# Kernel tuning notes

Measured on AMD Instinct MI355X. Metric: run time of the kernel, lower is better.

The kernel has to match this reference:

```python
import jax, jax.numpy as jnp
import numpy as np

BN_EPS = 1e-5

# Binary_a: sign forward, hard-tanh STE backward (grad zeroed where |x| >= 1)
@jax.custom_vjp
def binary_act(x):
    return jnp.sign(x)

def _ba_fwd(x):
    return jnp.sign(x), x

def _ba_bwd(x, g):
    return (jnp.where((x > -1.0) & (x < 1.0), g, 0.0),)

binary_act.defvjp(_ba_fwd, _ba_bwd)

# Binary_w: sign forward, identity STE backward
@jax.custom_vjp
def binary_w(x):
    return jnp.sign(x)

def _bw_fwd(x):
    return jnp.sign(x), None

def _bw_bwd(_, g):
    return (g,)

binary_w.defvjp(_bw_fwd, _bw_bwd)


def setup_inputs() -> dict:
    key = jax.random.key(0)
    k1, k2, k3 = jax.random.split(key, 3)
    B, Cin, Cout, H, Wd, K = 32, 256, 256, 56, 56, 3
    x = jax.random.normal(k1, (B, Cin, H, Wd), dtype=jnp.float32)
    weight = jax.random.normal(k2, (Cout, Cin, K, K), dtype=jnp.float32) * 0.05
    bias = jax.random.normal(k3, (Cout,), dtype=jnp.float32) * 0.01
    gamma = jnp.ones((Cout,), dtype=jnp.float32)
    beta = jnp.zeros((Cout,), dtype=jnp.float32)
    return {"x": x, "weight": weight, "bias": bias, "gamma": gamma, "beta": beta}


def reference(x, weight, bias, gamma, beta):
    # activation binarization (A=2)
    xb = binary_act(x)
    # weight quantization (W=2): mean-center over in-channel dim, clamp to [-1,1]
    # (done on .data in torch -> values change but no grad through this step)
    wc_val = jnp.clip(weight - jnp.mean(weight, axis=1, keepdims=True), -1.0, 1.0)
    wc = weight + jax.lax.stop_gradient(wc_val - weight)
    # per-output-filter scale alpha = E[|w|] over (in, kh, kw)
    alpha = jnp.mean(jnp.abs(wc), axis=(1, 2, 3), keepdims=True)
    wq = binary_w(wc) * alpha  # [O,I,K,K]
    # conv2d, stride 1, padding 1, groups 1
    y = jax.lax.conv_general_dilated(
        xb, wq, window_strides=(1, 1), padding=((1, 1), (1, 1)),
        dimension_numbers=("NCHW", "OIHW", "NCHW"))
    y = y + bias[None, :, None, None]
    # BatchNorm2d, training-mode forward (biased batch stats)
    mean = jnp.mean(y, axis=(0, 2, 3), keepdims=True)
    var = jnp.mean(jnp.square(y - mean), axis=(0, 2, 3), keepdims=True)
    y = (y - mean) * jax.lax.rsqrt(var + BN_EPS)
    y = y * gamma[None, :, None, None] + beta[None, :, None, None]
    # last_relu=1
    return jax.nn.relu(y)
```

## Files before the change

kernel.cpp:

```cpp
#include <hip/hip_runtime.h>
#include <stdint.h>

typedef unsigned long long u64;
typedef unsigned int u32;
typedef int v4i __attribute__((ext_vector_type(4)));
typedef int v16i __attribute__((ext_vector_type(16)));

#define B_    32
#define CIN   256
#define COUT  256
#define H_    56
#define W_    56
#define HW    3136
#define NPOS  100352
#define HBLK  28
#define NPACKBLK 784


__global__ __launch_bounds__(256) void k_prep(
    const float* __restrict__ x,
    const float* __restrict__ wgt,
    u64* __restrict__ xbits,
    int8_t* __restrict__ Bfrag,
    float* __restrict__ alpha,
    int* __restrict__ ssum,
    unsigned long long* __restrict__ qsum)
{
    const int tid = threadIdx.x;

    if (blockIdx.x < NPACKBLK) {
        const int j = blockIdx.x / 196;
        const int p2 = (blockIdx.x - j * 196) * 256 + tid;
        const int pos0 = p2 * 2;
        const int b = pos0 / HW;
        const int hw = pos0 - b * HW;
        const float* xp = x + (size_t)b * CIN * HW + (size_t)j * 64 * HW + hw;
        u64 b0 = 0, b1 = 0;
#pragma unroll 8
        for (int k = 0; k < 64; ++k) {
            const float2 v = *(const float2*)(xp + (size_t)k * HW);
            b0 |= (u64)(v.x > 0.0f) << k;
            b1 |= (u64)(v.y > 0.0f) << k;
        }
        xbits[(size_t)pos0 * 4 + j] = b0;
        xbits[(size_t)(pos0 + 1) * 4 + j] = b1;
        return;
    }

    const int o = blockIdx.x - NPACKBLK;
    const int i = tid;
    const int wave = i >> 6, lane = i & 63;
    __shared__ float sred[4][12];

    if (i == 0) { ssum[o] = 0; qsum[o] = 0ULL; }

    float w9[9];
#pragma unroll
    for (int t = 0; t < 9; ++t) w9[t] = wgt[(o * 256 + i) * 9 + t];

    float m[9];
#pragma unroll
    for (int t = 0; t < 9; ++t) m[t] = w9[t];
#pragma unroll
    for (int s = 1; s < 64; s <<= 1)
#pragma unroll
        for (int t = 0; t < 9; ++t) m[t] += __shfl_xor(m[t], s, 64);
    if (lane == 0) {
#pragma unroll
        for (int t = 0; t < 9; ++t) sred[wave][t] = m[t];
    }
    __syncthreads();
#pragma unroll
    for (int t = 0; t < 9; ++t)
        m[t] = (sred[0][t] + sred[1][t] + sred[2][t] + sred[3][t]) * (1.0f / 256.0f);

    float wc[9];
    float asum = 0.0f;
#pragma unroll
    for (int t = 0; t < 9; ++t) {
        float v = w9[t] - m[t];
        v = fminf(fmaxf(v, -1.0f), 1.0f);
        wc[t] = v;
        asum += fabsf(v);
    }
#pragma unroll
    for (int s = 1; s < 64; s <<= 1) asum += __shfl_xor(asum, s, 64);
    __syncthreads();
    if (lane == 0) sred[wave][9] = asum;
    __syncthreads();
    if (i == 0)
        alpha[o] = (sred[0][9] + sred[1][9] + sred[2][9] + sred[3][9]) * (1.0f / 2304.0f);

#pragma unroll
    for (int t = 0; t < 9; ++t) {
        const int8_t sv = (wc[t] > 0.0f) ? (int8_t)1 : (int8_t)-1;
        const size_t addr =
            ((size_t)((t * 8 + (i >> 5)) * 8 + (o >> 5)) * 64
             + (size_t)(((i >> 4) & 1) * 32 + (o & 31))) * 16 + (i & 15);
        Bfrag[addr] = sv;
    }
}

#define MFMA_I8(acc, a, b) \
    asm volatile("v_mfma_i32_32x32x32_i8 %0, %1, %2, %0" : "+a"(acc) : "v"(a), "v"(b))

__global__ __launch_bounds__(256, 2) void kc_mfma(
    const u64* __restrict__ xbits,
    const int8_t* __restrict__ Bfrag,
    short* __restrict__ S,
    int* __restrict__ ssum,
    unsigned long long* __restrict__ qsum)
{
    const int blk = blockIdx.x;
    const int b = blk / HBLK;
    const int h0 = (blk - b * HBLK) * 2;
    const int tid = threadIdx.x;

    __shared__ u32 ldsb[4 * 58 * 64];

    for (int it = tid; it < 4 * 58 * 16; it += 256) {
        const int r = it / 928;
        const int rem = it - r * 928;
        const int wp = rem >> 4;
        const int g = rem & 15;
        const int hr = h0 - 1 + r;
        const int w_in = wp - 1;
        const bool inb = (hr >= 0) && (hr < H_) && (w_in >= 0) && (w_in < W_);
        u32 chunk16 = 0;
        if (inb) {
            const u64 word = xbits[((size_t)(b * HW + hr * W_ + w_in)) * 4 + (g >> 2)];
            chunk16 = (u32)(word >> ((g & 3) * 16)) & 0xFFFFu;
        }
        u32 out4[4];
#pragma unroll
        for (int d = 0; d < 4; ++d) {
            const u32 nib = (chunk16 >> (4 * d)) & 0xFu;
            const u32 m1 = (nib * 0x00204081u) & 0x01010101u;
            const u32 inv = m1 ^ 0x01010101u;
            out4[d] = inb ? (0x01010101u ^ (inv * 0xFEu)) : 0u;
        }
        const int gs = (g + wp) & 15;
        u32* dst = &ldsb[((r * 58 + wp) << 6) + gs * 4];
        dst[0] = out4[0]; dst[1] = out4[1]; dst[2] = out4[2]; dst[3] = out4[3];
    }
    __syncthreads();

    const int m0 = tid & 31;
    const int lh = (tid >> 5) & 1;
    const int wv = tid >> 6;
    const int8_t* smem = (const int8_t*)ldsb;
    const int8_t* Bp = Bfrag + (size_t)(tid & 63) * 16;

    auto ldA = [&](int kk, int mt) -> v4i {
        const int tap = kk >> 3, s = kk & 7;
        const int dh = tap / 3;
        const int dw = tap - dh * 3;
        const int r = (mt >> 1) + dh;
        const int wpm = min((mt & 1) * 32 + m0 + dw, 57);
        const int gs = (2 * s + lh + wpm) & 15;
        const int addr = ((r * 58 + wpm) << 8) + (gs << 4);
        return *(const v4i*)(smem + addr);
    };
    auto ldB = [&](int kk, int ntl) -> v4i {
        const size_t off = (size_t)((kk * 8) + wv * 2 + ntl) * 1024;
        return *(const v4i*)(Bp + off);
    };

    v16i acc[4][2] = {};
    v4i A[4][2], Bb[2][2];

#pragma unroll
    for (int mt = 0; mt < 4; ++mt) A[mt][0] = ldA(0, mt);
    Bb[0][0] = ldB(0, 0);
    Bb[1][0] = ldB(0, 1);

#pragma unroll
    for (int kk = 0; kk < 72; ++kk) {
        const int cur = kk & 1, nxt = cur ^ 1;
        if (kk < 71) {
#pragma unroll
            for (int mt = 0; mt < 4; ++mt) A[mt][nxt] = ldA(kk + 1, mt);
            Bb[0][nxt] = ldB(kk + 1, 0);
            Bb[1][nxt] = ldB(kk + 1, 1);
        }
#pragma unroll
        for (int mt = 0; mt < 4; ++mt) {
            MFMA_I8(acc[mt][0], A[mt][cur], Bb[0][cur]);
            MFMA_I8(acc[mt][1], A[mt][cur], Bb[1][cur]);
        }
    }

    asm volatile("s_nop 7\n\ts_nop 7\n\ts_nop 7"
                 : "+a"(acc[0][0]), "+a"(acc[0][1]), "+a"(acc[1][0]), "+a"(acc[1][1]),
                   "+a"(acc[2][0]), "+a"(acc[2][1]), "+a"(acc[3][0]), "+a"(acc[3][1]));

    const int n0 = wv * 64 + m0;
    const int n1 = n0 + 32;
    int s0 = 0, s1 = 0, q0 = 0, q1 = 0;

#pragma unroll
    for (int mt = 0; mt < 4; ++mt) {
        const int h = h0 + (mt >> 1);
        const int rowbase = b * HW + h * W_ + ((mt & 1) << 5);
        const int nval = (mt & 1) ? 12 : 16;
#pragma unroll 16
        for (int reg = 0; reg < nval; ++reg) {
            const int m = (reg & 3) + ((reg >> 2) << 3) + (lh << 2);
            const int v0 = acc[mt][0][reg], v1 = acc[mt][1][reg];
            s0 += v0; q0 += v0 * v0; s1 += v1; q1 += v1 * v1;
            S[(size_t)(rowbase + m) * 256 + n0] = (short)v0;
            S[(size_t)(rowbase + m) * 256 + n1] = (short)v1;
        }
    }

    s0 += __shfl_xor(s0, 32, 64); q0 += __shfl_xor(q0, 32, 64);
    s1 += __shfl_xor(s1, 32, 64); q1 += __shfl_xor(q1, 32, 64);
    if (lh == 0) {
        atomicAdd(&ssum[n0], s0);
        atomicAdd(&qsum[n0], (unsigned long long)(long long)q0);
        atomicAdd(&ssum[n1], s1);
        atomicAdd(&qsum[n1], (unsigned long long)(long long)q1);
    }
}

__global__ __launch_bounds__(256) void kb_apply(
    const short* __restrict__ S,
    const int* __restrict__ ssum,
    const unsigned long long* __restrict__ qsum,
    const float* __restrict__ alpha,
    const float* __restrict__ gamma,
    const float* __restrict__ beta,
    float* __restrict__ out)
{
    const int blk = blockIdx.x;
    const int chunk = blk % 49;
    const int bcg = blk / 49;
    const int cg = bcg & 3;
    const int b = bcg >> 2;
    const int c0 = cg * 64;
    const int p0 = chunk * 64;
    const int tid = threadIdx.x;

    __shared__ float s_scale[64], s_shift[64];
    __shared__ u32 lds[64 * 33];

    if (tid < 64) {
        const int o = c0 + tid;
        const double N = (double)NPOS;
        double meanS = (double)ssum[o] / N;
        double varS = (double)qsum[o] / N - meanS * meanS;
        double a = (double)alpha[o];
        double rstd = 1.0 / sqrt(a * a * varS + 1e-5);
        double g = (double)gamma[o];
        s_scale[tid] = (float)(g * a * rstd);
        s_shift[tid] = (float)((double)beta[o] - g * a * meanS * rstd);
    }

    const u32* Sp = (const u32*)(S + ((size_t)b * HW + p0) * 256 + c0);
#pragma unroll
    for (int k = 0; k < 8; ++k) {
        const int idx = tid + k * 256;
        const int p = idx >> 5, cp = idx & 31;
        lds[p * 33 + cp] = Sp[p * 128 + cp];
    }
    __syncthreads();

    const int pl = tid & 63;
    const int ch4 = tid >> 6;
    const short* lss = (const short*)lds;
#pragma unroll
    for (int cc = 0; cc < 16; ++cc) {
        const int c = ch4 * 16 + cc;
        const float f = fmaxf(fmaf((float)lss[pl * 66 + c], s_scale[c], s_shift[c]), 0.0f);
        out[((size_t)(b * COUT + c0 + c)) * HW + p0 + pl] = f;
    }
}

extern "C" void kernel_launch(void* const* d_in, const int* in_sizes, int n_in,
                              void* d_out, int out_size, void* d_ws, size_t ws_size,
                              hipStream_t stream) {
    const float* x     = (const float*)d_in[0];
    const float* wgt   = (const float*)d_in[1];
    const float* gamma = (const float*)d_in[3];
    const float* beta  = (const float*)d_in[4];
    float* out = (float*)d_out;

    char* ws = (char*)d_ws;
    int8_t* Bfrag = (int8_t*)(ws + 0);
    float* alpha = (float*)(ws + 589824);
    int*   ssum  = (int*)(ws + 590848);
    unsigned long long* qsum = (unsigned long long*)(ws + 591872);
    u64*   xbits = (u64*)(ws + 593920);
    short* Sarr  = (short*)(ws + 3805184);

    k_prep<<<NPACKBLK + 256, 256, 0, stream>>>(x, wgt, xbits, Bfrag, alpha, ssum, qsum);
    kc_mfma<<<B_ * HBLK, 256, 0, stream>>>(xbits, Bfrag, Sarr, ssum, qsum);
    kb_apply<<<32 * 4 * 49, 256, 0, stream>>>(Sarr, ssum, qsum, alpha, gamma, beta, out);
}
```

Baseline: 279.5 us.

## Store intermediate conv sums channel-major and simplify BN apply kernel

The int16 intermediate S changes from position-major [pos][channel] to channel-major [channel][pos]. The MFMA epilogue now writes packed 4-short vectors and the BN/ReLU apply kernel streams contiguous 8-short vectors per (channel, batch), with no LDS transpose. The bit-packing kernel also handles four positions per thread with float4 loads instead of two. The risk is that the epilogue stores are now strided across channels, with 8-byte writes at 200KB channel stride, which may hurt write coalescing in the conv kernel.

```diff
diff --git a/kernel.cpp b/kernel.cpp
--- a/kernel.cpp
+++ b/kernel.cpp
@@ -5,6 +5,9 @@
 typedef unsigned int u32;
 typedef int v4i __attribute__((ext_vector_type(4)));
 typedef int v16i __attribute__((ext_vector_type(16)));
+typedef short s4v __attribute__((ext_vector_type(4)));
+typedef short s8v __attribute__((ext_vector_type(8)));
+typedef float f4v __attribute__((ext_vector_type(4)));
 
 #define B_    32
 #define CIN   256
@@ -14,7 +17,7 @@
 #define HW    3136
 #define NPOS  100352
 #define HBLK  28
-#define NPACKBLK 784
+#define NPACKBLK 392
 
 
 __global__ __launch_bounds__(256) void k_prep(
@@ -29,21 +32,25 @@
     const int tid = threadIdx.x;
 
     if (blockIdx.x < NPACKBLK) {
-        const int j = blockIdx.x / 196;
-        const int p2 = (blockIdx.x - j * 196) * 256 + tid;
-        const int pos0 = p2 * 2;
+        const int j = blockIdx.x / 98;
+        const int p4 = (blockIdx.x - j * 98) * 256 + tid;
+        const int pos0 = p4 * 4;
         const int b = pos0 / HW;
         const int hw = pos0 - b * HW;
         const float* xp = x + (size_t)b * CIN * HW + (size_t)j * 64 * HW + hw;
-        u64 b0 = 0, b1 = 0;
+        u64 b0 = 0, b1 = 0, b2 = 0, b3 = 0;
 #pragma unroll 8
         for (int k = 0; k < 64; ++k) {
-            const float2 v = *(const float2*)(xp + (size_t)k * HW);
+            const float4 v = *(const float4*)(xp + (size_t)k * HW);
             b0 |= (u64)(v.x > 0.0f) << k;
             b1 |= (u64)(v.y > 0.0f) << k;
+            b2 |= (u64)(v.z > 0.0f) << k;
+            b3 |= (u64)(v.w > 0.0f) << k;
         }
         xbits[(size_t)pos0 * 4 + j] = b0;
         xbits[(size_t)(pos0 + 1) * 4 + j] = b1;
+        xbits[(size_t)(pos0 + 2) * 4 + j] = b2;
+        xbits[(size_t)(pos0 + 3) * 4 + j] = b3;
         return;
     }
 
@@ -195,21 +202,26 @@
                    "+a"(acc[2][0]), "+a"(acc[2][1]), "+a"(acc[3][0]), "+a"(acc[3][1]));
 
     const int n0 = wv * 64 + m0;
-    const int n1 = n0 + 32;
     int s0 = 0, s1 = 0, q0 = 0, q1 = 0;
 
 #pragma unroll
     for (int mt = 0; mt < 4; ++mt) {
         const int h = h0 + (mt >> 1);
-        const int rowbase = b * HW + h * W_ + ((mt & 1) << 5);
-        const int nval = (mt & 1) ? 12 : 16;
-#pragma unroll 16
-        for (int reg = 0; reg < nval; ++reg) {
-            const int m = (reg & 3) + ((reg >> 2) << 3) + (lh << 2);
-            const int v0 = acc[mt][0][reg], v1 = acc[mt][1][reg];
-            s0 += v0; q0 += v0 * v0; s1 += v1; q1 += v1 * v1;
-            S[(size_t)(rowbase + m) * 256 + n0] = (short)v0;
-            S[(size_t)(rowbase + m) * 256 + n1] = (short)v1;
+        const size_t rowb = (size_t)b * HW + (size_t)h * W_ + ((mt & 1) << 5) + (lh << 2);
+        const int nq = (mt & 1) ? 3 : 4;
+#pragma unroll
+        for (int q = 0; q < nq; ++q) {
+            s4v pk0, pk1;
+#pragma unroll
+            for (int j = 0; j < 4; ++j) {
+                const int v0 = acc[mt][0][4 * q + j];
+                const int v1 = acc[mt][1][4 * q + j];
+                s0 += v0; q0 += v0 * v0; s1 += v1; q1 += v1 * v1;
+                pk0[j] = (short)v0;
+                pk1[j] = (short)v1;
+            }
+            *(s4v*)(S + (size_t)n0 * NPOS + rowb + 8 * q) = pk0;
+            *(s4v*)(S + (size_t)(n0 + 32) * NPOS + rowb + 8 * q) = pk1;
         }
     }
 
@@ -218,8 +230,8 @@
     if (lh == 0) {
         atomicAdd(&ssum[n0], s0);
         atomicAdd(&qsum[n0], (unsigned long long)(long long)q0);
-        atomicAdd(&ssum[n1], s1);
-        atomicAdd(&qsum[n1], (unsigned long long)(long long)q1);
+        atomicAdd(&ssum[n0 + 32], s1);
+        atomicAdd(&qsum[n0 + 32], (unsigned long long)(long long)q1);
     }
 }
 
@@ -233,46 +245,32 @@
     float* __restrict__ out)
 {
     const int blk = blockIdx.x;
-    const int chunk = blk % 49;
-    const int bcg = blk / 49;
-    const int cg = bcg & 3;
-    const int b = bcg >> 2;
-    const int c0 = cg * 64;
-    const int p0 = chunk * 64;
-    const int tid = threadIdx.x;
-
-    __shared__ float s_scale[64], s_shift[64];
-    __shared__ u32 lds[64 * 33];
-
-    if (tid < 64) {
-        const int o = c0 + tid;
-        const double N = (double)NPOS;
-        double meanS = (double)ssum[o] / N;
-        double varS = (double)qsum[o] / N - meanS * meanS;
-        double a = (double)alpha[o];
-        double rstd = 1.0 / sqrt(a * a * varS + 1e-5);
-        double g = (double)gamma[o];
-        s_scale[tid] = (float)(g * a * rstd);
-        s_shift[tid] = (float)((double)beta[o] - g * a * meanS * rstd);
-    }
-
-    const u32* Sp = (const u32*)(S + ((size_t)b * HW + p0) * 256 + c0);
-#pragma unroll
-    for (int k = 0; k < 8; ++k) {
-        const int idx = tid + k * 256;
-        const int p = idx >> 5, cp = idx & 31;
-        lds[p * 33 + cp] = Sp[p * 128 + cp];
-    }
-    __syncthreads();
-
-    const int pl = tid & 63;
-    const int ch4 = tid >> 6;
-    const short* lss = (const short*)lds;
-#pragma unroll
-    for (int cc = 0; cc < 16; ++cc) {
-        const int c = ch4 * 16 + cc;
-        const float f = fmaxf(fmaf((float)lss[pl * 66 + c], s_scale[c], s_shift[c]), 0.0f);
-        out[((size_t)(b * COUT + c0 + c)) * HW + p0 + pl] = f;
+    const int c = blk >> 5;
+    const int b = blk & 31;
+
+    const double N = (double)NPOS;
+    const double meanS = (double)ssum[c] / N;
+    const double varS = (double)qsum[c] / N - meanS * meanS;
+    const double a = (double)alpha[c];
+    const double rstd = 1.0 / sqrt(a * a * varS + 1e-5);
+    const double g = (double)gamma[c];
+    const float scale = (float)(g * a * rstd);
+    const float shift = (float)((double)beta[c] - g * a * meanS * rstd);
+
+    const s8v* src = (const s8v*)(S + (size_t)c * NPOS + (size_t)b * HW);
+    float* dst = out + ((size_t)(b * COUT + c)) * HW;
+
+    for (int idx = threadIdx.x; idx < HW / 8; idx += 256) {
+        const s8v v = src[idx];
+        f4v o0, o1;
+#pragma unroll
+        for (int j = 0; j < 4; ++j)
+            o0[j] = fmaxf(fmaf((float)v[j], scale, shift), 0.0f);
+#pragma unroll
+        for (int j = 0; j < 4; ++j)
+            o1[j] = fmaxf(fmaf((float)v[4 + j], scale, shift), 0.0f);
+        *(f4v*)(dst + idx * 8) = o0;
+        *(f4v*)(dst + idx * 8 + 4) = o1;
     }
 }
 
@@ -295,5 +293,5 @@
 
     k_prep<<<NPACKBLK + 256, 256, 0, stream>>>(x, wgt, xbits, Bfrag, alpha, ssum, qsum);
     kc_mfma<<<B_ * HBLK, 256, 0, stream>>>(xbits, Bfrag, Sarr, ssum, qsum);
-    kb_apply<<<32 * 4 * 49, 256, 0, stream>>>(Sarr, ssum, qsum, alpha, gamma, beta, out);
-}
+    kb_apply<<<COUT * B_, 256, 0, stream>>>(Sarr, ssum, qsum, alpha, gamma, beta, out);
+}
```

After: 286.9 us. 1.03x slower.
